# Optimization experiments

Measured on AMD Instinct MI355X. Metric: run time of the kernel, lower is better.

The kernel has to match this reference:

```python
import jax, jax.numpy as jnp
import numpy as np

B, T, H, NC = 64, 512, 1000, 2000
WV, PV, IV, TV, MV = 100000, 50, 5, 20, 500
FEAT = 300 + 4 * 50  # 500
EPS = 1e-5


def setup_inputs() -> dict:
    key = jax.random.key(0)
    ks = jax.random.split(key, 32)

    def emb(k, v, d):
        t = jax.random.normal(k, (v, d), jnp.float32) * 0.1
        return t.at[0].set(0.0)  # padding_idx=0

    def unif(k, shape, s):
        return jax.random.uniform(k, shape, jnp.float32, -s, s)

    s = 1.0 / np.sqrt(H)
    inp = {}
    inp['word_idxs'] = jax.random.randint(ks[0], (B, T), 0, WV)
    inp['pos_idxs'] = jax.random.randint(ks[1], (B, T), 0, PV)
    inp['iob_idxs'] = jax.random.randint(ks[2], (B, T), 0, IV)
    inp['type_idxs'] = jax.random.randint(ks[3], (B, T), 0, TV)
    inp['mention_idxs'] = jax.random.randint(ks[4], (B, T), 0, MV)
    lengths = jnp.sort(jax.random.randint(ks[5], (B,), 1, T + 1))[::-1]
    inp['lengths'] = lengths.at[0].set(T)  # descending, max == T
    inp['hidden'] = jnp.zeros((2, B, H), jnp.float32)
    inp['word_emb'] = emb(ks[6], WV, 300)
    inp['pos_emb'] = emb(ks[7], PV, 50)
    inp['iob_emb'] = emb(ks[8], IV, 50)
    inp['type_emb'] = emb(ks[9], TV, 50)
    inp['mention_emb'] = emb(ks[10], MV, 50)
    inp['w_ih_fwd'] = unif(ks[11], (3 * H, FEAT), s)
    inp['w_hh_fwd'] = unif(ks[12], (3 * H, H), s)
    inp['b_ih_fwd'] = unif(ks[13], (3 * H,), s)
    inp['b_hh_fwd'] = unif(ks[14], (3 * H,), s)
    inp['w_ih_bwd'] = unif(ks[15], (3 * H, FEAT), s)
    inp['w_hh_bwd'] = unif(ks[16], (3 * H, H), s)
    inp['b_ih_bwd'] = unif(ks[17], (3 * H,), s)
    inp['b_hh_bwd'] = unif(ks[18], (3 * H,), s)
    inp['lin_w'] = unif(ks[19], (NC, 2 * H), 1.0 / np.sqrt(2 * H))
    inp['lin_b'] = unif(ks[20], (NC,), 1.0 / np.sqrt(2 * H))
    inp['bn_gamma'] = 1.0 + 0.1 * jax.random.normal(ks[21], (NC,), jnp.float32)
    inp['bn_beta'] = 0.1 * jax.random.normal(ks[22], (NC,), jnp.float32)
    inp['bn_mean'] = 0.1 * jax.random.normal(ks[23], (NC,), jnp.float32)
    inp['bn_var'] = jax.random.uniform(ks[24], (NC,), jnp.float32, 0.5, 1.5)
    return inp


def _gru_dir(x_proj, mask, h0, w_hh, b_hh):
    """x_proj: [T,B,3H] precomputed input projections; mask: [T,B] validity."""
    def step(h, tm):
        xp, m = tm
        hp = h @ w_hh.T + b_hh  # [B,3H]
        xr, xz, xn = jnp.split(xp, 3, axis=-1)
        hr, hz, hn = jnp.split(hp, 3, axis=-1)
        r = jax.nn.sigmoid(xr + hr)
        z = jax.nn.sigmoid(xz + hz)
        n = jnp.tanh(xn + r * hn)
        h_new = (1.0 - z) * n + z * h
        h = jnp.where(m[:, None], h_new, h)  # freeze past sequence end (packed semantics)
        return h, None
    hT, _ = jax.lax.scan(step, h0, (x_proj, mask))
    return hT


def reference(word_idxs, pos_idxs, iob_idxs, type_idxs, mention_idxs, lengths, hidden,
              word_emb, pos_emb, iob_emb, type_emb, mention_emb,
              w_ih_fwd, w_hh_fwd, b_ih_fwd, b_hh_fwd,
              w_ih_bwd, w_hh_bwd, b_ih_bwd, b_hh_bwd,
              lin_w, lin_b, bn_gamma, bn_beta, bn_mean, bn_var):
    # multi-embedding concat -> [B,T,500]; eval mode: dropouts identity
    feat = jnp.concatenate([
        word_emb[word_idxs], pos_emb[pos_idxs], iob_emb[iob_idxs],
        type_emb[type_idxs], mention_emb[mention_idxs]], axis=-1)
    valid = (jnp.arange(T)[None, :] < lengths[:, None])  # [B,T]

    # forward direction
    xpf = jnp.einsum('btf,gf->tbg', feat, w_ih_fwd) + b_ih_fwd  # [T,B,3H]
    h_f = _gru_dir(xpf, valid.T, hidden[0], w_hh_fwd, b_hh_fwd)

    # backward direction: reverse the valid portion of each sequence
    rev_idx = jnp.clip(lengths[:, None] - 1 - jnp.arange(T)[None, :], 0, T - 1)  # [B,T]
    feat_r = jnp.take_along_axis(feat, rev_idx[:, :, None], axis=1)
    xpb = jnp.einsum('btf,gf->tbg', feat_r, w_ih_bwd) + b_ih_bwd
    h_b = _gru_dir(xpb, valid.T, hidden[1], w_hh_bwd, b_hh_bwd)

    h_cat = jnp.concatenate([h_f, h_b], axis=-1)  # [B,2H]
    logits = h_cat @ lin_w.T + lin_b
    out = bn_gamma * (logits - bn_mean) * jax.lax.rsqrt(bn_var + EPS) + bn_beta
    hidden_out = jnp.stack([h_f, h_b])  # [2,B,H] like PyTorch GRU final hidden
    return out, hidden_out
```

## Files before the change

### kernel.cpp

```cpp
#include <hip/hip_runtime.h>
#include <hip/hip_bf16.h>

typedef __attribute__((ext_vector_type(8))) short bf16x8;
typedef __attribute__((ext_vector_type(4))) float f32x4;

#define MFMA16(a,b,c) __builtin_amdgcn_mfma_f32_16x16x32_bf16((a),(b),(c),0,0,0)

__device__ __forceinline__ float sigmf(float x){ return 1.f/(1.f + __expf(-x)); }
__device__ __forceinline__ float tanh_fast(float x){
    float e = __expf(-2.f*fabsf(x));
    float t = (1.f-e)/(1.f+e);
    return x < 0.f ? -t : t;
}

#define AS1 __attribute__((address_space(1)))
#define AS3 __attribute__((address_space(3)))
__device__ __forceinline__ void gll16(const void* g, void* l) {
    __builtin_amdgcn_global_load_lds((const AS1 unsigned int*)g, (AS3 unsigned int*)l, 16, 0, 0);
}

__device__ __forceinline__ bf16x8 load16_asm(const __hip_bfloat16* p) {
    bf16x8 v;
    asm volatile("global_load_dwordx4 %0, %1, off" : "=v"(v) : "v"(p));
    return v;
}
__device__ __forceinline__ bf16x8 load16_sc(const __hip_bfloat16* p) {
    bf16x8 v;
    asm volatile("global_load_dwordx4 %0, %1, off sc0 sc1" : "=v"(v) : "v"(p) : "memory");
    return v;
}
__device__ __forceinline__ void store2_sc(__hip_bfloat16* p, float v) {
    __hip_bfloat16 b = __float2bfloat16(v);
    unsigned int u = *reinterpret_cast<unsigned short*>(&b);
    asm volatile("global_store_short %0, %1, off sc0 sc1" :: "v"(p), "v"(u) : "memory");
}
__device__ __forceinline__ unsigned poll_sc(const unsigned* p) {
    unsigned v;
    asm volatile("global_load_dword %0, %1, off sc0 sc1\n\ts_waitcnt vmcnt(0)"
                 : "=v"(v) : "v"(p) : "memory");
    return v;
}

#define B_   64
#define T_   512
#define H_   1000
#define HP   1024
#define G3   3072
#define NC_  2000
#define FEAT_C 500
#define FEAT_P 512
#define NROWS 32768

#define OFF_FEAT  ((size_t)0)
#define OFF_WIHF  (OFF_FEAT + 33554432ull)
#define OFF_WIHB  (OFF_WIHF + 3145728ull)
#define OFF_WHH   (OFF_WIHB + 3145728ull)
#define OFF_LINW  (OFF_WHH + 12582912ull)
#define OFF_BIHF  (OFF_LINW + 8192000ull)
#define OFF_BIHB  (OFF_BIHF + 12288ull)
#define OFF_BHH   (OFF_BIHB + 12288ull)
#define OFF_XP    (OFF_BHH + 24576ull)
#define OFF_HBF   (OFF_XP + 402653184ull)
#define OFF_HCAT  (OFF_HBF + 524288ull)
#define OFF_BAR   (OFF_HCAT + 262144ull)
#define WS_NEED   (OFF_BAR + 1024ull)

__global__ void cvt_pad_3h(const float* __restrict__ src, __hip_bfloat16* __restrict__ dst,
                           int C, int Cp) {
    size_t i = (size_t)blockIdx.x*blockDim.x + threadIdx.x;
    size_t total = (size_t)G3 * Cp;
    if (i >= total) return;
    int r = (int)(i / Cp), c = (int)(i % Cp);
    int chunk = r >> 10, j = r & 1023;
    float v = (j < H_ && c < C) ? src[((size_t)chunk*H_ + j)*C + c] : 0.f;
    dst[i] = __float2bfloat16(v);
}

__global__ void cvt_pad(const float* __restrict__ src, __hip_bfloat16* __restrict__ dst,
                        int R, int C, int Cp) {
    size_t i = (size_t)blockIdx.x*blockDim.x + threadIdx.x;
    size_t total = (size_t)R * Cp;
    if (i >= total) return;
    int r = (int)(i / Cp), c = (int)(i % Cp);
    float v = (c < C) ? src[(size_t)r*C + c] : 0.f;
    dst[i] = __float2bfloat16(v);
}

__global__ void pad_b3h(const float* __restrict__ src, float* __restrict__ dst) {
    int i = blockIdx.x*blockDim.x + threadIdx.x;
    if (i >= G3) return;
    int chunk = i >> 10, j = i & 1023;
    dst[i] = (j < H_) ? src[chunk*H_ + j] : 0.f;
}

__global__ __launch_bounds__(256)
void embed_k(const int* __restrict__ wi, const int* __restrict__ pi, const int* __restrict__ ii,
             const int* __restrict__ ti, const int* __restrict__ mi,
             const float* __restrict__ we, const float* __restrict__ pe, const float* __restrict__ ie,
             const float* __restrict__ te, const float* __restrict__ me,
             __hip_bfloat16* __restrict__ feat) {
    int r = blockIdx.x;
    int iw = wi[r], ip = pi[r], ib = ii[r], it = ti[r], im = mi[r];
    #pragma unroll
    for (int q = 0; q < 2; ++q) {
        int c = threadIdx.x + q*256;
        float v;
        if      (c < 300) v = we[(size_t)iw*300 + c];
        else if (c < 350) v = pe[ip*50 + (c-300)];
        else if (c < 400) v = ie[ib*50 + (c-350)];
        else if (c < 450) v = te[it*50 + (c-400)];
        else if (c < 500) v = me[im*50 + (c-450)];
        else              v = 0.f;
        feat[(size_t)r*FEAT_P + c] = __float2bfloat16(v);
    }
}

__global__ __launch_bounds__(256)
void gemm_xp(const __hip_bfloat16* __restrict__ feat,
             const __hip_bfloat16* __restrict__ W,
             const float* __restrict__ bias,
             const int* __restrict__ lengths,
             __hip_bfloat16* __restrict__ xp,
             int dir) {
    __shared__ char smem_raw[32768];
    __hip_bfloat16* As = (__hip_bfloat16*)smem_raw;
    __hip_bfloat16* Bs = (__hip_bfloat16*)(smem_raw + 16384);
    const int tid = threadIdx.x;
    const int wave = tid >> 6, lane = tid & 63;
    const int bm = blockIdx.x, bn = blockIdx.y;
    const int wm = wave >> 1, wn = wave & 1;

    int arow_src[4];
    #pragma unroll
    for (int q = 0; q < 4; ++q) {
        int flat = q*256 + tid;
        int row = flat >> 3;
        int r_g = bm*128 + row;
        int t = r_g >> 6, b = r_g & 63;
        int src_t;
        if (dir == 0) src_t = t;
        else { int L = lengths[b]; src_t = L - 1 - t; src_t = src_t < 0 ? 0 : src_t; }
        arow_src[q] = b*T_ + src_t;
    }

    f32x4 acc[4][4];
    #pragma unroll
    for (int i = 0; i < 4; ++i)
        #pragma unroll
        for (int j = 0; j < 4; ++j) acc[i][j] = (f32x4){0.f,0.f,0.f,0.f};

    for (int kt = 0; kt < 8; ++kt) {
        int k0 = kt*64;
        #pragma unroll
        for (int q = 0; q < 4; ++q) {
            int flat = q*256 + tid;
            int row = flat >> 3, c8 = flat & 7;
            gll16(feat + (size_t)arow_src[q]*FEAT_P + k0 + c8*8,
                  As + (q*256 + wave*64)*8);
            gll16(W + (size_t)(bn*128 + row)*FEAT_P + k0 + c8*8,
                  Bs + (q*256 + wave*64)*8);
        }
        __syncthreads();
        #pragma unroll
        for (int ks = 0; ks < 2; ++ks) {
            bf16x8 af[4], bfr[4];
            #pragma unroll
            for (int i = 0; i < 4; ++i)
                af[i] = *(const bf16x8*)(As + (wm*64 + i*16 + (lane&15))*64 + ks*32 + (lane>>4)*8);
            #pragma unroll
            for (int j = 0; j < 4; ++j)
                bfr[j] = *(const bf16x8*)(Bs + (wn*64 + j*16 + (lane&15))*64 + ks*32 + (lane>>4)*8);
            #pragma unroll
            for (int i = 0; i < 4; ++i)
                #pragma unroll
                for (int j = 0; j < 4; ++j)
                    acc[i][j] = MFMA16(af[i], bfr[j], acc[i][j]);
        }
        __syncthreads();
    }

    __hip_bfloat16* Cs = (__hip_bfloat16*)smem_raw;
    #pragma unroll
    for (int j = 0; j < 4; ++j) {
        int col_l = wn*64 + j*16 + (lane & 15);
        float bs = bias[bn*128 + col_l];
        #pragma unroll
        for (int i = 0; i < 4; ++i) {
            #pragma unroll
            for (int r = 0; r < 4; ++r) {
                int row_l = wm*64 + i*16 + (lane>>4)*4 + r;
                Cs[row_l*128 + col_l] = __float2bfloat16(acc[i][j][r] + bs);
            }
        }
    }
    __syncthreads();
    #pragma unroll
    for (int q = 0; q < 8; ++q) {
        int flat = q*256 + tid;
        int row = flat >> 4, c8 = flat & 15;
        bf16x8 v = *(const bf16x8*)(Cs + row*128 + c8*8);
        *(bf16x8*)(xp + (size_t)(bm*128 + row)*G3 + bn*128 + c8*8) = v;
    }
}

__global__ void init_h(const float* __restrict__ hidden, __hip_bfloat16* __restrict__ hbf) {
    int i = blockIdx.x*blockDim.x + threadIdx.x;
    if (i >= 2*B_*HP) return;
    int row = i >> 10, j = i & 1023;
    int dir = row >> 6, b = row & 63;
    float v = (j < H_) ? hidden[((size_t)dir*B_ + b)*H_ + j] : 0.f;
    __hip_bfloat16 bv = __float2bfloat16(v);
    hbf[i] = bv;
    hbf[2*B_*HP + i] = bv;
}

__global__ void bar_init(unsigned* bar) { if (threadIdx.x < 256) bar[threadIdx.x] = 0u; }

__global__ __launch_bounds__(512, 2)
void gru_persist(const __hip_bfloat16* __restrict__ whh,
                 const float* __restrict__ bhh,
                 const __hip_bfloat16* __restrict__ xp,
                 const int* __restrict__ lengths,
                 const float* __restrict__ hidden,
                 __hip_bfloat16* __restrict__ hbf,
                 __hip_bfloat16* __restrict__ hcat,
                 float* __restrict__ hid_o,
                 unsigned* __restrict__ bar) {
    __shared__ float part[2][4][3][256];
    const int blk = blockIdx.x;
    const int r8  = blk & 7, q8 = blk >> 3;
    const int g   = r8 >> 1;
    const int dir = g >> 1, bh = g & 1;
    const int ug  = q8*2 + (r8 & 1);
    const int w    = threadIdx.x >> 6;
    const int lane = threadIdx.x & 63;
    const int bg  = w >> 2;
    const int kh  = w & 3;
    const int u   = lane & 15;
    const int rg  = lane >> 4;

    const int j   = ug*16 + u;
    const int bA  = bh*32 + bg*16 + u;
    const int bF  = bh*32 + bg*16 + rg*4 + kh;
    const int myLen  = lengths[bF];
    const int lenBlk = lengths[bh*32];

    unsigned* cntp = bar + g*32;
    unsigned* flgp = bar + 128 + g*32;

    const float bhr = bhh[dir*G3 + j];
    const float bhz = bhh[dir*G3 + HP + j];
    const float bhn = bhh[dir*G3 + 2*HP + j];
    float hreg = (j < H_) ? hidden[((size_t)dir*B_ + bF)*H_ + j] : 0.f;

    bf16x8 wf0[8], wf1[8], wf2[8];
    {
        const __hip_bfloat16* wb = whh + (size_t)dir*G3*HP + (size_t)j*HP + kh*256 + rg*8;
        #pragma unroll
        for (int ks = 0; ks < 8; ++ks) {
            wf0[ks] = load16_asm(wb + ks*32);
            wf1[ks] = load16_asm(wb + (size_t)HP*HP + ks*32);
            wf2[ks] = load16_asm(wb + (size_t)2*HP*HP + ks*32);
        }
        asm volatile("s_waitcnt vmcnt(0)" ::: "memory");
        __builtin_amdgcn_sched_barrier(0);
    }

    const size_t hrowA = (size_t)(dir*B_ + bA)*HP + kh*256 + rg*8;
    const size_t hidxF = (size_t)(dir*B_ + bF)*HP + j;
    const size_t xbase = (size_t)dir*NROWS*G3 + (size_t)bF*G3 + j;

    for (int t = 0; t < lenBlk; ++t) {
        const int cur = t & 1, prev = cur ^ 1;
        const __hip_bfloat16* xr_p = xp + xbase + (size_t)t*B_*G3;
        float xr = __bfloat162float(xr_p[0]);
        float xz = __bfloat162float(xr_p[HP]);
        float xn = __bfloat162float(xr_p[2*HP]);
        const __hip_bfloat16* ha = hbf + (size_t)prev*2*B_*HP + hrowA;
        bf16x8 af[8];
        #pragma unroll
        for (int ks = 0; ks < 8; ++ks) af[ks] = load16_sc(ha + ks*32);
        asm volatile("s_waitcnt vmcnt(0)" ::: "memory");
        __builtin_amdgcn_sched_barrier(0);

        f32x4 a0 = {0.f,0.f,0.f,0.f}, a1 = {0.f,0.f,0.f,0.f}, a2 = {0.f,0.f,0.f,0.f};
        #pragma unroll
        for (int ks = 0; ks < 8; ++ks) {
            a0 = MFMA16(af[ks], wf0[ks], a0);
            a1 = MFMA16(af[ks], wf1[ks], a1);
            a2 = MFMA16(af[ks], wf2[ks], a2);
        }
        *(f32x4*)&part[bg][kh][0][lane*4] = a0;
        *(f32x4*)&part[bg][kh][1][lane*4] = a1;
        *(f32x4*)&part[bg][kh][2][lane*4] = a2;
        __syncthreads();
        float sr = 0.f, sz = 0.f, sn = 0.f;
        #pragma unroll
        for (int q = 0; q < 4; ++q) {
            sr += part[bg][q][0][lane*4 + kh];
            sz += part[bg][q][1][lane*4 + kh];
            sn += part[bg][q][2][lane*4 + kh];
        }
        float rr = sigmf(xr + sr + bhr);
        float zz = sigmf(xz + sz + bhz);
        float nn = tanh_fast(xn + rr*(sn + bhn));
        float hnew = (t < myLen) ? ((1.f - zz)*nn + zz*hreg) : hreg;
        hreg = hnew;
        store2_sc(hbf + (size_t)cur*2*B_*HP + hidxF, hnew);
        asm volatile("s_waitcnt vmcnt(0)" ::: "memory");
        __syncthreads();

        if (t + 1 < lenBlk) {
            if (threadIdx.x == 0) {
                unsigned a = atomicAdd(cntp, 1u);
                if (a == 64u*(unsigned)(t+1) - 1u) {
                    atomicAdd(flgp, 1u);
                } else {
                    while (poll_sc(flgp) <= (unsigned)t)
                        __builtin_amdgcn_s_sleep(2);
                }
            }
            __syncthreads();
        }
    }

    if (j < H_) {
        hid_o[((size_t)dir*B_ + bF)*H_ + j] = hreg;
        hcat[(size_t)bF*2048 + dir*H_ + j] = __float2bfloat16(hreg);
    }
}

__global__ __launch_bounds__(256)
void lin_bn_k(const __hip_bfloat16* __restrict__ hcat,
              const __hip_bfloat16* __restrict__ linw,
              const float* __restrict__ lin_b, const float* __restrict__ gamma,
              const float* __restrict__ beta, const float* __restrict__ mean,
              const float* __restrict__ var,
              float* __restrict__ out) {
    __shared__ __hip_bfloat16 wlds[16*2056];
    const int n0 = blockIdx.x*16;
    const int tid = threadIdx.x;
    #pragma unroll
    for (int q = 0; q < 16; ++q) {
        int flat8 = q*256 + tid;
        int row = flat8 >> 8, c8 = flat8 & 255;
        bf16x8 v = *(const bf16x8*)(linw + (size_t)(n0+row)*2048 + c8*8);
        *(bf16x8*)(wlds + row*2056 + c8*8) = v;
    }
    __syncthreads();
    const int wave = tid >> 6, lane = tid & 63;
    const int mrow = wave*16 + (lane & 15);
    f32x4 acc = {0.f,0.f,0.f,0.f};
    for (int ks = 0; ks < 64; ++ks) {
        bf16x8 a = *(const bf16x8*)(hcat + (size_t)mrow*2048 + ks*32 + (lane>>4)*8);
        bf16x8 b = *(const bf16x8*)(wlds + (lane&15)*2056 + ks*32 + (lane>>4)*8);
        acc = MFMA16(a, b, acc);
    }
    const int c = n0 + (lane & 15);
    const float g = gamma[c], bt = beta[c], mn = mean[c], lb = lin_b[c];
    const float iv = rsqrtf(var[c] + 1e-5f);
    #pragma unroll
    for (int r = 0; r < 4; ++r) {
        int b_ = wave*16 + (lane>>4)*4 + r;
        float logit = acc[r] + lb;
        out[(size_t)b_*NC_ + c] = g*(logit - mn)*iv + bt;
    }
}

extern "C" void kernel_launch(void* const* d_in, const int* in_sizes, int n_in,
                              void* d_out, int out_size, void* d_ws, size_t ws_size,
                              hipStream_t stream) {
    const int*   wi      = (const int*)d_in[0];
    const int*   pi      = (const int*)d_in[1];
    const int*   ii      = (const int*)d_in[2];
    const int*   ti      = (const int*)d_in[3];
    const int*   mi      = (const int*)d_in[4];
    const int*   lengths = (const int*)d_in[5];
    const float* hidden  = (const float*)d_in[6];
    const float* we      = (const float*)d_in[7];
    const float* pe      = (const float*)d_in[8];
    const float* ie      = (const float*)d_in[9];
    const float* te      = (const float*)d_in[10];
    const float* me      = (const float*)d_in[11];
    const float* w_ih_f  = (const float*)d_in[12];
    const float* w_hh_f  = (const float*)d_in[13];
    const float* b_ih_f  = (const float*)d_in[14];
    const float* b_hh_f  = (const float*)d_in[15];
    const float* w_ih_b  = (const float*)d_in[16];
    const float* w_hh_b  = (const float*)d_in[17];
    const float* b_ih_b  = (const float*)d_in[18];
    const float* b_hh_b  = (const float*)d_in[19];
    const float* lin_w   = (const float*)d_in[20];
    const float* lin_b   = (const float*)d_in[21];
    const float* gamma   = (const float*)d_in[22];
    const float* beta    = (const float*)d_in[23];
    const float* mean    = (const float*)d_in[24];
    const float* var     = (const float*)d_in[25];
    float* out = (float*)d_out;

    if (ws_size < WS_NEED) return;

    char* ws = (char*)d_ws;
    __hip_bfloat16* FEAT = (__hip_bfloat16*)(ws + OFF_FEAT);
    __hip_bfloat16* WIHF = (__hip_bfloat16*)(ws + OFF_WIHF);
    __hip_bfloat16* WIHB = (__hip_bfloat16*)(ws + OFF_WIHB);
    __hip_bfloat16* WHH  = (__hip_bfloat16*)(ws + OFF_WHH);
    __hip_bfloat16* LINW = (__hip_bfloat16*)(ws + OFF_LINW);
    float* BIHF = (float*)(ws + OFF_BIHF);
    float* BIHB = (float*)(ws + OFF_BIHB);
    float* BHH  = (float*)(ws + OFF_BHH);
    __hip_bfloat16* XP   = (__hip_bfloat16*)(ws + OFF_XP);
    __hip_bfloat16* HBF  = (__hip_bfloat16*)(ws + OFF_HBF);
    __hip_bfloat16* HCAT = (__hip_bfloat16*)(ws + OFF_HCAT);
    unsigned* BAR = (unsigned*)(ws + OFF_BAR);
    float* HIDO = out + (size_t)B_*NC_;

    cvt_pad_3h<<<(G3*512 + 255)/256, 256, 0, stream>>>(w_ih_f, WIHF, FEAT_C, FEAT_P);
    cvt_pad_3h<<<(G3*512 + 255)/256, 256, 0, stream>>>(w_ih_b, WIHB, FEAT_C, FEAT_P);
    cvt_pad_3h<<<(G3*1024 + 255)/256, 256, 0, stream>>>(w_hh_f, WHH, H_, HP);
    cvt_pad_3h<<<(G3*1024 + 255)/256, 256, 0, stream>>>(w_hh_b, WHH + (size_t)G3*HP, H_, HP);
    cvt_pad<<<(NC_*2048 + 255)/256, 256, 0, stream>>>(lin_w, LINW, NC_, NC_, 2048);
    pad_b3h<<<(G3 + 255)/256, 256, 0, stream>>>(b_ih_f, BIHF);
    pad_b3h<<<(G3 + 255)/256, 256, 0, stream>>>(b_ih_b, BIHB);
    pad_b3h<<<(G3 + 255)/256, 256, 0, stream>>>(b_hh_f, BHH);
    pad_b3h<<<(G3 + 255)/256, 256, 0, stream>>>(b_hh_b, BHH + G3);

    embed_k<<<NROWS, 256, 0, stream>>>(wi, pi, ii, ti, mi, we, pe, ie, te, me, FEAT);

    dim3 gg(NROWS/128, G3/128);
    gemm_xp<<<gg, 256, 0, stream>>>(FEAT, WIHF, BIHF, lengths, XP, 0);
    gemm_xp<<<gg, 256, 0, stream>>>(FEAT, WIHB, BIHB, lengths, XP + (size_t)NROWS*G3, 1);

    init_h<<<(2*B_*HP + 255)/256, 256, 0, stream>>>(hidden, HBF);
    bar_init<<<1, 256, 0, stream>>>(BAR);
    {
        void* args[] = { (void*)&WHH, (void*)&BHH, (void*)&XP, (void*)&lengths,
                         (void*)&hidden, (void*)&HBF, (void*)&HCAT, (void*)&HIDO, (void*)&BAR };
        hipLaunchCooperativeKernel((const void*)gru_persist, dim3(256), dim3(512),
                                   args, 0, stream);
    }

    lin_bn_k<<<NC_/16, 256, 0, stream>>>(HCAT, LINW, lin_b, gamma, beta, mean, var, out);
}
```

Baseline: 3.158 ms.

## Replace atomic counter barrier with per-block flag slots and prefetch x projections

The inter-block barrier in the persistent GRU kernel now has each block write its step number to its own slot, and one wave polls all 64 slots in parallel with a wave-wide vote. This replaces the serialized atomicAdd counter plus flag. The next timestep's input projections are also prefetched with raw loads issued after the MFMAs, so their latency hides behind the reduction and barrier. The new barrier depends on cross-block store visibility through sc0 sc1, and the launch bounds were rewritten as explicit attributes.

```diff
diff --git a/kernel.cpp b/kernel.cpp
--- a/kernel.cpp
+++ b/kernel.cpp
@@ -34,10 +34,18 @@
     unsigned int u = *reinterpret_cast<unsigned short*>(&b);
     asm volatile("global_store_short %0, %1, off sc0 sc1" :: "v"(p), "v"(u) : "memory");
 }
+__device__ __forceinline__ void store4_sc(unsigned* p, unsigned v) {
+    asm volatile("global_store_dword %0, %1, off sc0 sc1" :: "v"(p), "v"(v) : "memory");
+}
 __device__ __forceinline__ unsigned poll_sc(const unsigned* p) {
     unsigned v;
     asm volatile("global_load_dword %0, %1, off sc0 sc1\n\ts_waitcnt vmcnt(0)"
                  : "=v"(v) : "v"(p) : "memory");
+    return v;
+}
+__device__ __forceinline__ unsigned ld2_g(const __hip_bfloat16* p) {
+    unsigned v;
+    asm volatile("global_load_ushort %0, %1, off" : "=v"(v) : "v"(p));
     return v;
 }
 
@@ -216,7 +224,7 @@
 
 __global__ void bar_init(unsigned* bar) { if (threadIdx.x < 256) bar[threadIdx.x] = 0u; }
 
-__global__ __launch_bounds__(512, 2)
+__global__ __attribute__((amdgpu_flat_work_group_size(512,512), amdgpu_waves_per_eu(2,2)))
 void gru_persist(const __hip_bfloat16* __restrict__ whh,
                  const float* __restrict__ bhh,
                  const __hip_bfloat16* __restrict__ xp,
@@ -245,8 +253,7 @@
     const int myLen  = lengths[bF];
     const int lenBlk = lengths[bh*32];
 
-    unsigned* cntp = bar + g*32;
-    unsigned* flgp = bar + 128 + g*32;
+    unsigned* slots = bar + g*64;
 
     const float bhr = bhh[dir*G3 + j];
     const float bhz = bhh[dir*G3 + HP + j];
@@ -270,12 +277,15 @@
     const size_t hidxF = (size_t)(dir*B_ + bF)*HP + j;
     const size_t xbase = (size_t)dir*NROWS*G3 + (size_t)bF*G3 + j;
 
+    unsigned pxr, pxz, pxn;
+    {
+        const __hip_bfloat16* x0 = xp + xbase;
+        pxr = ld2_g(x0); pxz = ld2_g(x0 + HP); pxn = ld2_g(x0 + 2*HP);
+        asm volatile("s_waitcnt vmcnt(0)" ::: "memory");
+    }
+
     for (int t = 0; t < lenBlk; ++t) {
         const int cur = t & 1, prev = cur ^ 1;
-        const __hip_bfloat16* xr_p = xp + xbase + (size_t)t*B_*G3;
-        float xr = __bfloat162float(xr_p[0]);
-        float xz = __bfloat162float(xr_p[HP]);
-        float xn = __bfloat162float(xr_p[2*HP]);
         const __hip_bfloat16* ha = hbf + (size_t)prev*2*B_*HP + hrowA;
         bf16x8 af[8];
         #pragma unroll
@@ -290,6 +300,17 @@
             a1 = MFMA16(af[ks], wf1[ks], a1);
             a2 = MFMA16(af[ks], wf2[ks], a2);
         }
+
+        float xr = __uint_as_float(pxr << 16);
+        float xz = __uint_as_float(pxz << 16);
+        float xn = __uint_as_float(pxn << 16);
+
+        {
+            int tn = (t + 1 < lenBlk) ? t + 1 : t;
+            const __hip_bfloat16* xnp = xp + xbase + (size_t)tn*B_*G3;
+            pxr = ld2_g(xnp); pxz = ld2_g(xnp + HP); pxn = ld2_g(xnp + 2*HP);
+        }
+
         *(f32x4*)&part[bg][kh][0][lane*4] = a0;
         *(f32x4*)&part[bg][kh][1][lane*4] = a1;
         *(f32x4*)&part[bg][kh][2][lane*4] = a2;
@@ -311,13 +332,13 @@
         __syncthreads();
 
         if (t + 1 < lenBlk) {
-            if (threadIdx.x == 0) {
-                unsigned a = atomicAdd(cntp, 1u);
-                if (a == 64u*(unsigned)(t+1) - 1u) {
-                    atomicAdd(flgp, 1u);
-                } else {
-                    while (poll_sc(flgp) <= (unsigned)t)
-                        __builtin_amdgcn_s_sleep(2);
+            if (w == 0) {
+                if (lane == 0) store4_sc(&slots[ug], (unsigned)(t + 1));
+                const unsigned tgt = (unsigned)(t + 1);
+                for (;;) {
+                    unsigned v = poll_sc(slots + lane);
+                    if (__all((int)(v >= tgt))) break;
+                    __builtin_amdgcn_s_sleep(1);
                 }
             }
             __syncthreads();
```

After: 3.490 ms. 1.1x slower.
